# Kernel tuning notes

Measured on AMD Instinct MI355X. Metric: run time of the kernel, lower is better.

Reference implementation:

```python
import jax, jax.numpy as jnp
import numpy as np

B, CIN, H, W = 4, 256, 64, 64
COUT = CIN // 2  # 128
EPS = 1e-5


def setup_inputs() -> dict:
    key = jax.random.key(0)
    ks = jax.random.split(key, 10)
    s_in = 1.0 / np.sqrt(CIN)
    s_out = 1.0 / np.sqrt(COUT)
    return {
        "x": jax.random.normal(ks[0], (B, CIN, H, W), dtype=jnp.float32),
        "Wq": jax.random.uniform(ks[1], (COUT, CIN), jnp.float32, -s_in, s_in),
        "bq": jax.random.uniform(ks[2], (COUT,), jnp.float32, -s_in, s_in),
        "Wk": jax.random.uniform(ks[3], (COUT, CIN), jnp.float32, -s_in, s_in),
        "bk": jax.random.uniform(ks[4], (COUT,), jnp.float32, -s_in, s_in),
        "Wv": jax.random.uniform(ks[5], (COUT, CIN), jnp.float32, -s_in, s_in),
        "bv": jax.random.uniform(ks[6], (COUT,), jnp.float32, -s_in, s_in),
        "Ww": jax.random.uniform(ks[7], (CIN, COUT), jnp.float32, -s_out, s_out),
        "bw": jax.random.uniform(ks[8], (CIN,), jnp.float32, -s_out, s_out),
        "bn_gamma": jnp.ones((CIN,), jnp.float32),
        "bn_beta": jnp.zeros((CIN,), jnp.float32),
        "bn_mean": jnp.zeros((CIN,), jnp.float32),
        "bn_var": jnp.ones((CIN,), jnp.float32),
    }


def reference(x, Wq, bq, Wk, bk, Wv, bv, Ww, bw, bn_gamma, bn_beta, bn_mean, bn_var):
    b, c, h, w = x.shape
    n = h * w
    xf = x.reshape(b, c, n)  # [B, Cin, N]
    # 1x1 convs == channel-mixing matmuls on flattened spatial dim
    q = jnp.einsum("oc,bcn->bon", Wq, xf) + bq[None, :, None]  # [B, Cout, N]
    k = jnp.einsum("oc,bcn->bon", Wk, xf) + bk[None, :, None]
    v = jnp.einsum("oc,bcn->bon", Wv, xf) + bv[None, :, None]
    # f = k^T @ q  (no scaling, as in the original)
    f = jnp.einsum("bcn,bcm->bnm", k, q)  # [B, N, N]
    f = jax.nn.softmax(f, axis=-1)
    # y = v @ f
    y = jnp.einsum("bcn,bnm->bcm", v, f)  # [B, Cout, N]
    # output 1x1 conv + eval-mode BatchNorm + residual
    z = jnp.einsum("oc,bcn->bon", Ww, y) + bw[None, :, None]  # [B, Cin, N]
    inv = bn_gamma / jnp.sqrt(bn_var + EPS)
    z = z * inv[None, :, None] + (bn_beta - bn_mean * inv)[None, :, None]
    return z.reshape(b, c, h, w) + x
```

## Files before the change

kernel.cpp:

```cpp
#include <hip/hip_runtime.h>
#include <hip/hip_bf16.h>

#define BATCH 4
#define CIN   256
#define CMID  128
#define NPOS  4096
#define EPS   1e-5f

typedef __bf16 bf16;
typedef __attribute__((ext_vector_type(8))) __bf16 bf16x8;
typedef __attribute__((ext_vector_type(4))) __bf16 bf16x4;
typedef __attribute__((ext_vector_type(4))) float  f32x4;

#define MFMA16(a, b, c) __builtin_amdgcn_mfma_f32_16x16x32_bf16((a), (b), (c), 0, 0, 0)

#define GLDS(gsrc, ldst) \
    __builtin_amdgcn_global_load_lds( \
        (const __attribute__((address_space(1))) void*)(gsrc), \
        (__attribute__((address_space(3))) void*)(ldst), 16, 0, 0)

__device__ __forceinline__ int swz128(int row, int colb) {
    return row * 128 + ((((colb >> 4) ^ (row & 7)) << 4) | (colb & 15));
}
__device__ __forceinline__ int swz256(int row, int colb) {
    return row * 256 + ((((colb >> 4) ^ (row & 7)) << 4) | (colb & 15));
}

__global__ __launch_bounds__(256) void kt_transpose(const float* __restrict__ x,
                                                    bf16* __restrict__ xT) {
    __shared__ float tile[64][65];
    int n0 = blockIdx.x * 64, c0 = blockIdx.y * 64, b = blockIdx.z;
    const float* xp = x + (size_t)b * CIN * NPOS;
    int t = threadIdx.x;
    int lr = t >> 4;
    int lc4 = (t & 15) * 4;
    for (int p = 0; p < 4; ++p) {
        int c = lr + p * 16;
        f32x4 v = *reinterpret_cast<const f32x4*>(xp + (size_t)(c0 + c) * NPOS + n0 + lc4);
        tile[c][lc4 + 0] = v[0]; tile[c][lc4 + 1] = v[1];
        tile[c][lc4 + 2] = v[2]; tile[c][lc4 + 3] = v[3];
    }
    __syncthreads();
    bf16* xtp = xT + (size_t)b * NPOS * CIN;
    int cc = (t & 15) * 4;
    for (int p = 0; p < 4; ++p) {
        int n = (t >> 4) + p * 16;
        bf16x4 o;
        o[0] = (bf16)tile[cc + 0][n]; o[1] = (bf16)tile[cc + 1][n];
        o[2] = (bf16)tile[cc + 2][n]; o[3] = (bf16)tile[cc + 3][n];
        *reinterpret_cast<bf16x4*>(xtp + (size_t)(n0 + n) * CIN + c0 + cc) = o;
    }
}

__global__ __launch_bounds__(256) void k_qkv(
    const float* __restrict__ Wq, const float* __restrict__ Wk, const float* __restrict__ Wv,
    const float* __restrict__ bq, const float* __restrict__ bk, const float* __restrict__ bv,
    const bf16* __restrict__ xT, bf16* __restrict__ qT, bf16* __restrict__ kT,
    bf16* __restrict__ vC) {
    __shared__ __align__(16) char a_lds[128 * 128];
    __shared__ __align__(16) char b_lds[128 * 128];
    int n0 = blockIdx.x * 128, which = blockIdx.y, b = blockIdx.z;
    const float* W    = which == 0 ? Wq : (which == 1 ? Wk : Wv);
    const float* bias = which == 0 ? bq : (which == 1 ? bk : bv);
    int t = threadIdx.x, lane = t & 63, w = t >> 6, wy = w >> 1, wx = w & 1;
    const bf16* xb = xT + (size_t)b * NPOS * CIN;

    f32x4 acc[4][4] = {};
    for (int k0 = 0; k0 < 256; k0 += 64) {
        __syncthreads();
        for (int i = 0; i < 8; ++i) {
            int idx = t + i * 256;
            int row = idx >> 4, c4 = (idx & 15) * 4;
            f32x4 v = *reinterpret_cast<const f32x4*>(W + (size_t)row * CIN + k0 + c4);
            bf16x4 o; o[0] = (bf16)v[0]; o[1] = (bf16)v[1]; o[2] = (bf16)v[2]; o[3] = (bf16)v[3];
            *reinterpret_cast<bf16x4*>(a_lds + swz128(row, c4 * 2)) = o;
        }
        for (int i = 0; i < 4; ++i) {
            int idx = t + i * 256;
            int row = idx >> 3, cb = (idx & 7) * 16;
            bf16x8 vv = *reinterpret_cast<const bf16x8*>(xb + (size_t)(n0 + row) * CIN + k0 + cb / 2);
            *reinterpret_cast<bf16x8*>(b_lds + swz128(row, cb)) = vv;
        }
        __syncthreads();
        for (int ks = 0; ks < 2; ++ks) {
            int kb = ks * 64 + (lane >> 4) * 16;
            bf16x8 af[4], bfr[4];
            for (int i = 0; i < 4; ++i)
                af[i] = *reinterpret_cast<const bf16x8*>(a_lds + swz128(wy * 64 + i * 16 + (lane & 15), kb));
            for (int j = 0; j < 4; ++j)
                bfr[j] = *reinterpret_cast<const bf16x8*>(b_lds + swz128(wx * 64 + j * 16 + (lane & 15), kb));
            for (int i = 0; i < 4; ++i)
                for (int j = 0; j < 4; ++j)
                    acc[i][j] = MFMA16(af[i], bfr[j], acc[i][j]);
        }
    }
    int rg = lane >> 4, cl = lane & 15;
    for (int i = 0; i < 4; ++i) {
        int ch0 = wy * 64 + i * 16 + rg * 4;
        f32x4 bv4 = *reinterpret_cast<const f32x4*>(bias + ch0);
        for (int j = 0; j < 4; ++j) {
            int n = n0 + wx * 64 + j * 16 + cl;
            f32x4 d = acc[i][j];
            for (int r = 0; r < 4; ++r) d[r] += bv4[r];
            if (which == 2) {
                for (int r = 0; r < 4; ++r)
                    vC[((size_t)b * CMID + ch0 + r) * NPOS + n] = (bf16)d[r];
            } else {
                bf16x4 o; o[0] = (bf16)d[0]; o[1] = (bf16)d[1]; o[2] = (bf16)d[2]; o[3] = (bf16)d[3];
                bf16* dst = (which == 0 ? qT : kT);
                *reinterpret_cast<bf16x4*>(dst + ((size_t)b * NPOS + n) * CMID + ch0) = o;
            }
        }
    }
}

__global__ __launch_bounds__(256, 4) void k_zrow(const bf16* __restrict__ qT,
                                                 const bf16* __restrict__ kT,
                                                 float* __restrict__ zpart) {
    __shared__ __align__(16) char q_lds[2][64 * 256];
    int n0 = blockIdx.x * 128, mq = blockIdx.y, b = blockIdx.z;
    int t = threadIdx.x, lane = t & 63, w = t >> 6;
    int cl = lane & 15, g = lane >> 4;
    const bf16* qb = qT + (size_t)b * NPOS * CMID;
    const bf16* kb = kT + (size_t)b * NPOS * CMID;

    auto stage_q = [&](int buf, int m0) {
        #pragma unroll
        for (int i = 0; i < 4; ++i) {
            int lc = (w * 4 + i) * 64 + lane;
            int r = lc >> 4, p = lc & 15;
            GLDS(qb + (size_t)(m0 + r) * CMID + ((p ^ (r & 7)) << 3),
                 q_lds[buf] + (w * 4 + i) * 1024);
        }
    };

    bf16x8 kreg[2][4];
    for (int jn = 0; jn < 2; ++jn)
        for (int ks = 0; ks < 4; ++ks)
            kreg[jn][ks] = *reinterpret_cast<const bf16x8*>(
                kb + (size_t)(n0 + w * 32 + jn * 16 + cl) * CMID + ks * 32 + g * 8);

    int mbeg = mq * (NPOS / 8);
    stage_q(0, mbeg);
    asm volatile("s_waitcnt vmcnt(0)" ::: "memory");
    __syncthreads();
    int cur = 0;
    float zacc[2] = {0.f, 0.f};
    for (int m0 = mbeg; m0 < mbeg + NPOS / 8; m0 += 64) {
        if (m0 + 64 < mbeg + NPOS / 8) stage_q(cur ^ 1, m0 + 64);
        f32x4 acc[4][2] = {};
        for (int ks = 0; ks < 4; ++ks) {
            bf16x8 qf[4];
            for (int im = 0; im < 4; ++im)
                qf[im] = *reinterpret_cast<const bf16x8*>(q_lds[cur] + swz256(im * 16 + cl, ks * 64 + g * 16));
            for (int im = 0; im < 4; ++im)
                for (int jn = 0; jn < 2; ++jn)
                    acc[im][jn] = MFMA16(qf[im], kreg[jn][ks], acc[im][jn]);
        }
        for (int im = 0; im < 4; ++im)
            for (int jn = 0; jn < 2; ++jn)
                for (int r = 0; r < 4; ++r)
                    zacc[jn] += __expf(acc[im][jn][r]);
        __syncthreads();
        cur ^= 1;
    }
    for (int jn = 0; jn < 2; ++jn) {
        zacc[jn] += __shfl_xor(zacc[jn], 16);
        zacc[jn] += __shfl_xor(zacc[jn], 32);
    }
    if (g == 0) {
        float* zp = zpart + ((size_t)mq * BATCH + b) * NPOS;
        zp[n0 + w * 32 + cl]      = zacc[0];
        zp[n0 + w * 32 + 16 + cl] = zacc[1];
    }
}

__global__ __launch_bounds__(256) void k_rcp(const float* __restrict__ zpart,
                                             float* __restrict__ invZ) {
    int i = (blockIdx.x * 256 + threadIdx.x) * 4;
    f32x4 s = {0.f, 0.f, 0.f, 0.f};
    for (int p = 0; p < 8; ++p) {
        f32x4 a = *reinterpret_cast<const f32x4*>(zpart + (size_t)p * BATCH * NPOS + i);
        for (int r = 0; r < 4; ++r) s[r] += a[r];
    }
    f32x4 o;
    for (int r = 0; r < 4; ++r) o[r] = 1.f / s[r];
    *reinterpret_cast<f32x4*>(invZ + i) = o;
}

__global__ __launch_bounds__(256, 2) void k_attn(const bf16* __restrict__ qT,
                                                 const bf16* __restrict__ kT,
                                                 const bf16* __restrict__ vC,
                                                 const float* __restrict__ invZ,
                                                 bf16* __restrict__ ypA,
                                                 bf16* __restrict__ ypB) {
    __shared__ __align__(16) char k_lds[2][64 * 256];
    __shared__ __align__(16) char v_lds[2][128 * 128];
    __shared__ __align__(16) char p_lds[128 * 128];
    int m0 = blockIdx.x * 128, nq = blockIdx.y, b = blockIdx.z;
    int t = threadIdx.x, lane = t & 63, w = t >> 6;
    int cl = lane & 15, g = lane >> 4;
    const bf16* qb = qT + (size_t)b * NPOS * CMID;
    const bf16* kb = kT + (size_t)b * NPOS * CMID;
    const bf16* vb = vC + (size_t)b * CMID * NPOS;
    const float* izb = invZ + (size_t)b * NPOS;

    auto stage_kv = [&](int buf, int n0) {
        #pragma unroll
        for (int i = 0; i < 4; ++i) {
            int lc = (w * 4 + i) * 64 + lane;
            int kr = lc >> 4, kp = lc & 15;
            GLDS(kb + (size_t)(n0 + kr) * CMID + ((kp ^ (kr & 7)) << 3),
                 k_lds[buf] + (w * 4 + i) * 1024);
            int vr = lc >> 3, vp = lc & 7;
            GLDS(vb + (size_t)vr * NPOS + n0 + ((vp ^ (vr & 7)) << 3),
                 v_lds[buf] + (w * 4 + i) * 1024);
        }
    };

    bf16x8 qreg[2][4];
    for (int jm = 0; jm < 2; ++jm)
        for (int ks = 0; ks < 4; ++ks)
            qreg[jm][ks] = *reinterpret_cast<const bf16x8*>(
                qb + (size_t)(m0 + w * 32 + jm * 16 + cl) * CMID + ks * 32 + g * 8);

    f32x4 acc2[8][2] = {};
    int nbeg = nq * (NPOS / 4);
    stage_kv(0, nbeg);
    asm volatile("s_waitcnt vmcnt(0)" ::: "memory");
    __syncthreads();
    int cur = 0;
    for (int s = 0; s < NPOS / 4 / 64; ++s) {
        int n0 = nbeg + s * 64;
        if (s + 1 < NPOS / 4 / 64) stage_kv(cur ^ 1, n0 + 64);
        f32x4 iz[4];
        for (int in = 0; in < 4; ++in)
            iz[in] = *reinterpret_cast<const f32x4*>(izb + n0 + in * 16 + g * 4);
        f32x4 acc1[4][2] = {};
        for (int ks = 0; ks < 4; ++ks) {
            bf16x8 kf[4];
            for (int in = 0; in < 4; ++in)
                kf[in] = *reinterpret_cast<const bf16x8*>(k_lds[cur] + swz256(in * 16 + cl, ks * 64 + g * 16));
            for (int in = 0; in < 4; ++in)
                for (int jm = 0; jm < 2; ++jm)
                    acc1[in][jm] = MFMA16(kf[in], qreg[jm][ks], acc1[in][jm]);
        }
        for (int in = 0; in < 4; ++in)
            for (int jm = 0; jm < 2; ++jm) {
                bf16x4 o;
                for (int r = 0; r < 4; ++r) o[r] = (bf16)(__expf(acc1[in][jm][r]) * iz[in][r]);
                *reinterpret_cast<bf16x4*>(p_lds + swz128(w * 32 + jm * 16 + cl, in * 32 + g * 8)) = o;
            }
        __syncthreads();
        for (int ks = 0; ks < 2; ++ks) {
            bf16x8 af[8], vf[2];
            for (int i = 0; i < 8; ++i)
                af[i] = *reinterpret_cast<const bf16x8*>(p_lds + swz128(i * 16 + cl, ks * 64 + g * 16));
            for (int j = 0; j < 2; ++j)
                vf[j] = *reinterpret_cast<const bf16x8*>(v_lds[cur] + swz128(w * 32 + j * 16 + cl, ks * 64 + g * 16));
            for (int i = 0; i < 8; ++i)
                for (int j = 0; j < 2; ++j)
                    acc2[i][j] = MFMA16(af[i], vf[j], acc2[i][j]);
        }
        __syncthreads();
        cur ^= 1;
    }
    bf16* yb = ((nq & 2) ? ypB : ypA) + ((size_t)(nq & 1) * BATCH + b) * NPOS * CMID
             + (size_t)m0 * CMID;
    for (int i = 0; i < 8; ++i)
        for (int j = 0; j < 2; ++j) {
            int c = w * 32 + j * 16 + cl;
            for (int r = 0; r < 4; ++r) {
                int m = i * 16 + g * 4 + r;
                yb[(size_t)m * CMID + c] = (bf16)acc2[i][j][r];
            }
        }
}

__global__ __launch_bounds__(256) void k_out(
    const float* __restrict__ Ww, const float* __restrict__ bw,
    const float* __restrict__ gamma, const float* __restrict__ beta,
    const float* __restrict__ mean, const float* __restrict__ var,
    const bf16* __restrict__ ypA, const bf16* __restrict__ ypB,
    const float* __restrict__ x, float* __restrict__ out) {
    __shared__ __align__(16) char a_lds[128 * 128];
    __shared__ __align__(16) char b_lds[128 * 128];
    int m0 = blockIdx.x * 128, o0 = blockIdx.y * 128, b = blockIdx.z;
    int t = threadIdx.x, lane = t & 63, w = t >> 6, wy = w >> 1, wx = w & 1;
    size_t boff = (size_t)b * NPOS * CMID;
    const bf16* y0 = ypA + boff;
    const bf16* y1 = ypA + (size_t)BATCH * NPOS * CMID + boff;
    const bf16* y2 = ypB + boff;
    const bf16* y3 = ypB + (size_t)BATCH * NPOS * CMID + boff;
    f32x4 acc[4][4] = {};
    for (int k0 = 0; k0 < 128; k0 += 64) {
        __syncthreads();
        for (int i = 0; i < 8; ++i) {
            int idx = t + i * 256, row = idx >> 4, c4 = (idx & 15) * 4;
            f32x4 v = *reinterpret_cast<const f32x4*>(Ww + (size_t)(o0 + row) * CMID + k0 + c4);
            bf16x4 o; o[0] = (bf16)v[0]; o[1] = (bf16)v[1]; o[2] = (bf16)v[2]; o[3] = (bf16)v[3];
            *reinterpret_cast<bf16x4*>(a_lds + swz128(row, c4 * 2)) = o;
        }
        for (int i = 0; i < 8; ++i) {
            int idx = t + i * 256, row = idx >> 4, c4 = (idx & 15) * 4;
            size_t yoff = (size_t)(m0 + row) * CMID + k0 + c4;
            bf16x4 a0 = *reinterpret_cast<const bf16x4*>(y0 + yoff);
            bf16x4 a1 = *reinterpret_cast<const bf16x4*>(y1 + yoff);
            bf16x4 a2 = *reinterpret_cast<const bf16x4*>(y2 + yoff);
            bf16x4 a3 = *reinterpret_cast<const bf16x4*>(y3 + yoff);
            bf16x4 o;
            for (int r = 0; r < 4; ++r)
                o[r] = (bf16)((float)a0[r] + (float)a1[r] + (float)a2[r] + (float)a3[r]);
            *reinterpret_cast<bf16x4*>(b_lds + swz128(row, c4 * 2)) = o;
        }
        __syncthreads();
        for (int ks = 0; ks < 2; ++ks) {
            int kb = ks * 64 + (lane >> 4) * 16;
            bf16x8 af[4], bfr[4];
            for (int i = 0; i < 4; ++i)
                af[i] = *reinterpret_cast<const bf16x8*>(a_lds + swz128(wy * 64 + i * 16 + (lane & 15), kb));
            for (int j = 0; j < 4; ++j)
                bfr[j] = *reinterpret_cast<const bf16x8*>(b_lds + swz128(wx * 64 + j * 16 + (lane & 15), kb));
            for (int i = 0; i < 4; ++i)
                for (int j = 0; j < 4; ++j)
                    acc[i][j] = MFMA16(af[i], bfr[j], acc[i][j]);
        }
    }
    int rg = lane >> 4, cl = lane & 15;
    const float* xb = x + (size_t)b * CIN * NPOS;
    float* ob = out + (size_t)b * CIN * NPOS;
    for (int i = 0; i < 4; ++i) {
        int och0 = o0 + wy * 64 + i * 16 + rg * 4;
        f32x4 g  = *reinterpret_cast<const f32x4*>(gamma + och0);
        f32x4 be = *reinterpret_cast<const f32x4*>(beta + och0);
        f32x4 mu = *reinterpret_cast<const f32x4*>(mean + och0);
        f32x4 va = *reinterpret_cast<const f32x4*>(var + och0);
        f32x4 bb = *reinterpret_cast<const f32x4*>(bw + och0);
        float invv[4], addv[4];
        for (int r = 0; r < 4; ++r) {
            invv[r] = g[r] / sqrtf(va[r] + EPS);
            addv[r] = be[r] - mu[r] * invv[r];
        }
        for (int j = 0; j < 4; ++j) {
            int m = m0 + wx * 64 + j * 16 + cl;
            for (int r = 0; r < 4; ++r) {
                float z = (acc[i][j][r] + bb[r]) * invv[r] + addv[r];
                ob[(size_t)(och0 + r) * NPOS + m] = z + xb[(size_t)(och0 + r) * NPOS + m];
            }
        }
    }
}

extern "C" void kernel_launch(void* const* d_in, const int* in_sizes, int n_in,
                              void* d_out, int out_size, void* d_ws, size_t ws_size,
                              hipStream_t stream) {
    const float* x     = (const float*)d_in[0];
    const float* Wq    = (const float*)d_in[1];
    const float* bq    = (const float*)d_in[2];
    const float* Wk    = (const float*)d_in[3];
    const float* bk    = (const float*)d_in[4];
    const float* Wv    = (const float*)d_in[5];
    const float* bv    = (const float*)d_in[6];
    const float* Ww    = (const float*)d_in[7];
    const float* bw    = (const float*)d_in[8];
    const float* gamma = (const float*)d_in[9];
    const float* beta  = (const float*)d_in[10];
    const float* mean  = (const float*)d_in[11];
    const float* var   = (const float*)d_in[12];
    float* out = (float*)d_out;

    char* ws = (char*)d_ws;
    char* regionA = ws;                    ws += (size_t)BATCH * NPOS * CIN * 2;
    bf16* qT = (bf16*)ws;                  ws += (size_t)BATCH * NPOS * CMID * 2;
    bf16* kT = (bf16*)ws;                  ws += (size_t)BATCH * NPOS * CMID * 2;
    bf16* vC = (bf16*)ws;                  ws += (size_t)BATCH * NPOS * CMID * 2;
    bf16* ypB = (bf16*)ws;                 ws += (size_t)2 * BATCH * NPOS * CMID * 2;
    float* zpart = (float*)ws;             ws += (size_t)8 * BATCH * NPOS * 4;
    float* invZ = (float*)ws;
    bf16* xT  = (bf16*)regionA;
    bf16* ypA = (bf16*)regionA;

    kt_transpose<<<dim3(NPOS / 64, CIN / 64, BATCH), 256, 0, stream>>>(x, xT);
    k_qkv<<<dim3(NPOS / 128, 3, BATCH), 256, 0, stream>>>(Wq, Wk, Wv, bq, bk, bv, xT, qT, kT, vC);
    k_zrow<<<dim3(NPOS / 128, 8, BATCH), 256, 0, stream>>>(qT, kT, zpart);
    k_rcp<<<dim3(BATCH * NPOS / 1024), 256, 0, stream>>>(zpart, invZ);
    k_attn<<<dim3(NPOS / 128, 4, BATCH), 256, 0, stream>>>(qT, kT, vC, invZ, ypA, ypB);
    k_out<<<dim3(NPOS / 128, 2, BATCH), 256, 0, stream>>>(Ww, bw, gamma, beta, mean, var, ypA, ypB, x, out);
}
```

Before: 101.3 us.

## Fold softmax normalizer into V and make PV stage warp-local to drop barrier

Adds a small kernel that scales V in place by the per-key reciprocal softmax sums, so the attention kernel no longer loads invZ or multiplies each exp by it. The PV matmul is repartitioned so each warp consumes only the P rows it wrote (its own 32 query positions across all 128 channels). That removes the block-wide barrier between writing P and reading it. The cost is an extra kernel launch plus a read-modify-write of V, and a second bf16 rounding of V.

```diff
diff --git a/kernel.cpp b/kernel.cpp
--- a/kernel.cpp
+++ b/kernel.cpp
@@ -188,10 +188,26 @@
     *reinterpret_cast<f32x4*>(invZ + i) = o;
 }
 
+__global__ __launch_bounds__(256) void k_vscale(bf16* __restrict__ vC,
+                                                const float* __restrict__ invZ) {
+    int idx = blockIdx.x * 256 + threadIdx.x;
+    int b = idx >> 16;
+    int n8 = idx & (NPOS / 8 - 1);
+    bf16x8 v = *reinterpret_cast<const bf16x8*>(vC + (size_t)idx * 8);
+    const float* iz = invZ + (size_t)b * NPOS + n8 * 8;
+    f32x4 i0 = *reinterpret_cast<const f32x4*>(iz);
+    f32x4 i1 = *reinterpret_cast<const f32x4*>(iz + 4);
+    bf16x8 o;
+    for (int r = 0; r < 4; ++r) {
+        o[r]     = (bf16)((float)v[r]     * i0[r]);
+        o[r + 4] = (bf16)((float)v[r + 4] * i1[r]);
+    }
+    *reinterpret_cast<bf16x8*>(vC + (size_t)idx * 8) = o;
+}
+
 __global__ __launch_bounds__(256, 2) void k_attn(const bf16* __restrict__ qT,
                                                  const bf16* __restrict__ kT,
-                                                 const bf16* __restrict__ vC,
-                                                 const float* __restrict__ invZ,
+                                                 const bf16* __restrict__ vS,
                                                  bf16* __restrict__ ypA,
                                                  bf16* __restrict__ ypB) {
     __shared__ __align__(16) char k_lds[2][64 * 256];
@@ -202,8 +218,7 @@
     int cl = lane & 15, g = lane >> 4;
     const bf16* qb = qT + (size_t)b * NPOS * CMID;
     const bf16* kb = kT + (size_t)b * NPOS * CMID;
-    const bf16* vb = vC + (size_t)b * CMID * NPOS;
-    const float* izb = invZ + (size_t)b * NPOS;
+    const bf16* vb = vS + (size_t)b * CMID * NPOS;
 
     auto stage_kv = [&](int buf, int n0) {
         #pragma unroll
@@ -224,7 +239,7 @@
             qreg[jm][ks] = *reinterpret_cast<const bf16x8*>(
                 qb + (size_t)(m0 + w * 32 + jm * 16 + cl) * CMID + ks * 32 + g * 8);
 
-    f32x4 acc2[8][2] = {};
+    f32x4 acc2[2][8] = {};
     int nbeg = nq * (NPOS / 4);
     stage_kv(0, nbeg);
     asm volatile("s_waitcnt vmcnt(0)" ::: "memory");
@@ -233,9 +248,6 @@
     for (int s = 0; s < NPOS / 4 / 64; ++s) {
         int n0 = nbeg + s * 64;
         if (s + 1 < NPOS / 4 / 64) stage_kv(cur ^ 1, n0 + 64);
-        f32x4 iz[4];
-        for (int in = 0; in < 4; ++in)
-            iz[in] = *reinterpret_cast<const f32x4*>(izb + n0 + in * 16 + g * 4);
         f32x4 acc1[4][2] = {};
         for (int ks = 0; ks < 4; ++ks) {
             bf16x8 kf[4];
@@ -248,31 +260,30 @@
         for (int in = 0; in < 4; ++in)
             for (int jm = 0; jm < 2; ++jm) {
                 bf16x4 o;
-                for (int r = 0; r < 4; ++r) o[r] = (bf16)(__expf(acc1[in][jm][r]) * iz[in][r]);
+                for (int r = 0; r < 4; ++r) o[r] = (bf16)__expf(acc1[in][jm][r]);
                 *reinterpret_cast<bf16x4*>(p_lds + swz128(w * 32 + jm * 16 + cl, in * 32 + g * 8)) = o;
             }
-        __syncthreads();
-        for (int ks = 0; ks < 2; ++ks) {
-            bf16x8 af[8], vf[2];
-            for (int i = 0; i < 8; ++i)
-                af[i] = *reinterpret_cast<const bf16x8*>(p_lds + swz128(i * 16 + cl, ks * 64 + g * 16));
-            for (int j = 0; j < 2; ++j)
-                vf[j] = *reinterpret_cast<const bf16x8*>(v_lds[cur] + swz128(w * 32 + j * 16 + cl, ks * 64 + g * 16));
-            for (int i = 0; i < 8; ++i)
-                for (int j = 0; j < 2; ++j)
-                    acc2[i][j] = MFMA16(af[i], vf[j], acc2[i][j]);
+        for (int s32 = 0; s32 < 2; ++s32) {
+            bf16x8 af[2], vf[8];
+            for (int jm = 0; jm < 2; ++jm)
+                af[jm] = *reinterpret_cast<const bf16x8*>(p_lds + swz128(w * 32 + jm * 16 + cl, s32 * 64 + g * 16));
+            for (int j = 0; j < 8; ++j)
+                vf[j] = *reinterpret_cast<const bf16x8*>(v_lds[cur] + swz128(j * 16 + cl, s32 * 64 + g * 16));
+            for (int jm = 0; jm < 2; ++jm)
+                for (int j = 0; j < 8; ++j)
+                    acc2[jm][j] = MFMA16(af[jm], vf[j], acc2[jm][j]);
         }
         __syncthreads();
         cur ^= 1;
     }
     bf16* yb = ((nq & 2) ? ypB : ypA) + ((size_t)(nq & 1) * BATCH + b) * NPOS * CMID
              + (size_t)m0 * CMID;
-    for (int i = 0; i < 8; ++i)
-        for (int j = 0; j < 2; ++j) {
-            int c = w * 32 + j * 16 + cl;
+    for (int jm = 0; jm < 2; ++jm)
+        for (int j = 0; j < 8; ++j) {
+            int c = j * 16 + cl;
             for (int r = 0; r < 4; ++r) {
-                int m = i * 16 + g * 4 + r;
-                yb[(size_t)m * CMID + c] = (bf16)acc2[i][j][r];
+                int m = w * 32 + jm * 16 + g * 4 + r;
+                yb[(size_t)m * CMID + c] = (bf16)acc2[jm][j][r];
             }
         }
 }
@@ -384,6 +395,7 @@
     k_qkv<<<dim3(NPOS / 128, 3, BATCH), 256, 0, stream>>>(Wq, Wk, Wv, bq, bk, bv, xT, qT, kT, vC);
     k_zrow<<<dim3(NPOS / 128, 8, BATCH), 256, 0, stream>>>(qT, kT, zpart);
     k_rcp<<<dim3(BATCH * NPOS / 1024), 256, 0, stream>>>(zpart, invZ);
-    k_attn<<<dim3(NPOS / 128, 4, BATCH), 256, 0, stream>>>(qT, kT, vC, invZ, ypA, ypB);
+    k_vscale<<<dim3(BATCH * CMID * NPOS / 8 / 256), 256, 0, stream>>>(vC, invZ);
+    k_attn<<<dim3(NPOS / 128, 4, BATCH), 256, 0, stream>>>(qT, kT, vC, ypA, ypB);
     k_out<<<dim3(NPOS / 128, 2, BATCH), 256, 0, stream>>>(Ww, bw, gamma, beta, mean, var, ypA, ypB, x, out);
 }
```

After: 99.81 us. No clear change (-1.5%).
